# Optimization experiments

Measured on AMD Instinct MI355X. Metric: run time of the kernel, lower is better.

The kernel has to match this reference:

```python
import jax, jax.numpy as jnp
import numpy as np

V = 30522   # bert-base-uncased vocab size
B, S, D, J, K = 2, 512, 768, 12, 4
NUM_LABELS = 7


def setup_inputs() -> dict:
    key = jax.random.key(0)
    ks = jax.random.split(key, 9)
    return {
        "sequence_output": jax.random.normal(ks[0], (B, S, D), jnp.float32),
        "input_ids": jax.random.randint(ks[1], (B, S), 0, V),
        "neighbors": jax.random.randint(ks[2], (B, S, J, K), 0, V),
        "W_mlp": jax.random.normal(ks[3], (J * D, 13 * D), jnp.float32) * 0.02,
        "b_mlp": jnp.zeros((J * D,), jnp.float32),
        "W_attn": jax.random.normal(ks[4], (D, 2 * D), jnp.float32) * 0.02,
        "b_attn": jnp.zeros((D,), jnp.float32),
        "W_cls": jax.random.normal(ks[5], (NUM_LABELS, 2 * D), jnp.float32) * 0.02,
        "b_cls": jnp.zeros((NUM_LABELS,), jnp.float32),
    }


def _gather_neighbors(sequence_output, input_ids, neighbors):
    """Replicates the dict-based gather-sum. The torch dict persists ACROSS
    batch elements (it is never reset), with later positions overwriting
    earlier ones (last occurrence wins). We carry a [V,D] table + presence
    mask through a scan over the batch dim."""
    pos = jnp.arange(S, dtype=jnp.int32)

    def step(carry, xs):
        table, present = carry            # [V,D], [V] bool
        ids, seq, nb = xs                 # [S], [S,D], [S,J,K]
        # last occurrence index of each vocab id in this example (-1 if absent)
        last_idx = jnp.full((V,), -1, jnp.int32).at[ids].max(pos)
        found = last_idx >= 0
        table = jnp.where(found[:, None],
                          seq[jnp.clip(last_idx, 0, S - 1)], table)
        present = present | found
        # sum neighbor embeddings that are present in the dictionary
        emb = jnp.where(present[nb][..., None], table[nb], 0.0).sum(axis=2)  # [S,J,D]
        return (table, present), emb

    init = (jnp.zeros((V, D), sequence_output.dtype), jnp.zeros((V,), bool))
    _, fn = jax.lax.scan(step, init, (input_ids, sequence_output, neighbors))
    return fn                              # [B,S,J,D]


def reference(sequence_output, input_ids, neighbors,
              W_mlp, b_mlp, W_attn, b_attn, W_cls, b_cls):
    fn = _gather_neighbors(sequence_output, input_ids, neighbors)  # [B,S,J,D]
    n_flat = fn.reshape(B, S, J * D)
    # gated MLP: rij = [row ; neighbors], g = sigmoid(W rij), c' = g * n
    rij = jnp.concatenate([sequence_output, n_flat], axis=-1)      # [B,S,13D]
    g = jax.nn.sigmoid(jnp.einsum('bsf,gf->bsg', rij, W_mlp) + b_mlp)
    c = (g * n_flat).reshape(B, S, J, D)                           # [B,S,J,D]
    # Luong-style attention: query = token embedding, context = gated neighbors
    scores = jnp.einsum('bsd,bsjd->bsj', sequence_output, c)
    attn = jax.nn.softmax(scores, axis=-1)
    mix = jnp.einsum('bsj,bsjd->bsd', attn, c)                     # [B,S,D]
    combined = jnp.concatenate([mix, sequence_output], axis=-1)    # [B,S,2D]
    attn_out = jnp.tanh(jnp.einsum('bsf,df->bsd', combined, W_attn) + b_attn)
    final = jnp.concatenate([sequence_output, attn_out], axis=-1)  # [B,S,2D]
    # dropout is identity at inference
    logits = jnp.einsum('bsf,lf->bsl', final, W_cls) + b_cls       # [B,S,7]
    return logits
```

## Files before the change

kernel.cpp:

```cpp
#include <hip/hip_runtime.h>
#include <hip/hip_bf16.h>

#define V_PAD  30528
#define S_LEN  512
#define D_DIM  768
#define J_N    12
#define M_ROWS 1024
#define K_MLP  9984
#define N_MLP  9216
#define K_ATT  1536
#define N_ATT  768
#define N_LBL  7

using bf16x8 = __attribute__((ext_vector_type(8))) __bf16;
using f32x4  = __attribute__((ext_vector_type(4))) float;

__device__ __forceinline__ unsigned short f2bf(float f) {
  union { float f; unsigned int u; } c; c.f = f;
  unsigned int u = c.u;
  return (unsigned short)((u + 0x7fffu + ((u >> 16) & 1u)) >> 16);
}
__device__ __forceinline__ float bf2f(unsigned short h) {
  union { unsigned int u; float f; } c; c.u = (unsigned int)h << 16; return c.f;
}

__global__ __launch_bounds__(256)
void cvt_bf16_kernel(const float* __restrict__ in, unsigned short* __restrict__ out) {
  size_t i = (size_t)blockIdx.x * 256 + threadIdx.x;
  const float4 f0 = ((const float4*)in)[i * 2];
  const float4 f1 = ((const float4*)in)[i * 2 + 1];
  union { unsigned short h[8]; uint4 q; } pk;
  pk.h[0] = f2bf(f0.x); pk.h[1] = f2bf(f0.y); pk.h[2] = f2bf(f0.z); pk.h[3] = f2bf(f0.w);
  pk.h[4] = f2bf(f1.x); pk.h[5] = f2bf(f1.y); pk.h[6] = f2bf(f1.z); pk.h[7] = f2bf(f1.w);
  ((uint4*)out)[i] = pk.q;
}

__global__ void build_tables_kernel(const int* __restrict__ ids,
                                    int* __restrict__ last0,
                                    int* __restrict__ last01) {
  int p = blockIdx.x * 256 + threadIdx.x;
  if (p < M_ROWS) {
    int id = ids[p];
    atomicMax(&last01[id], p);
    if (p < S_LEN) atomicMax(&last0[id], p);
  }
}

__global__ __launch_bounds__(256) void seqrij_kernel(const float* __restrict__ seq,
                                                     unsigned short* __restrict__ rij) {
  int bs = blockIdx.x;
  for (int d = threadIdx.x; d < D_DIM; d += 256)
    rij[(size_t)bs * K_MLP + d] = f2bf(seq[(size_t)bs * D_DIM + d]);
}

template <bool WRITE_NFLAT>
__global__ __launch_bounds__(192)
void gather_kernel(const float* __restrict__ seq, const int* __restrict__ nbr,
                   const int* __restrict__ last0, const int* __restrict__ last01,
                   float* __restrict__ nflat, unsigned short* __restrict__ rij) {
  const int bsj = blockIdx.x;
  const int j  = bsj % J_N;
  const int bs = bsj / J_N;
  const int b  = bs >> 9;
  const int* nb = nbr + (size_t)bsj * 4;
  const int* tab = (b == 0) ? last0 : last01;
  const int s0 = tab[nb[0]], s1 = tab[nb[1]], s2 = tab[nb[2]], s3 = tab[nb[3]];
  const int d4 = threadIdx.x;
  float4 a = {0.f, 0.f, 0.f, 0.f};
  if (s0 >= 0) { float4 v = ((const float4*)(seq + (size_t)s0 * D_DIM))[d4]; a.x += v.x; a.y += v.y; a.z += v.z; a.w += v.w; }
  if (s1 >= 0) { float4 v = ((const float4*)(seq + (size_t)s1 * D_DIM))[d4]; a.x += v.x; a.y += v.y; a.z += v.z; a.w += v.w; }
  if (s2 >= 0) { float4 v = ((const float4*)(seq + (size_t)s2 * D_DIM))[d4]; a.x += v.x; a.y += v.y; a.z += v.z; a.w += v.w; }
  if (s3 >= 0) { float4 v = ((const float4*)(seq + (size_t)s3 * D_DIM))[d4]; a.x += v.x; a.y += v.y; a.z += v.z; a.w += v.w; }
  union { unsigned short h[4]; unsigned long long q; } pk;
  pk.h[0] = f2bf(a.x); pk.h[1] = f2bf(a.y); pk.h[2] = f2bf(a.z); pk.h[3] = f2bf(a.w);
  *(unsigned long long*)(rij + (size_t)bs * K_MLP + D_DIM + j * D_DIM + d4 * 4) = pk.q;
  if (WRITE_NFLAT)
    ((float4*)(nflat + (size_t)bs * N_MLP + j * D_DIM))[d4] = a;
}

template <int MODE, int TM, int TN, bool BF16B, bool SWZ>
__global__ __launch_bounds__(256)
void gemm_nt_kernel(const unsigned short* __restrict__ A,
                    const void* __restrict__ Wv,
                    const float* __restrict__ bias,
                    float* __restrict__ nflat_c,
                    float* __restrict__ outp,
                    int K, int N, int kchunk) {
  constexpr int FM = TM / 32;
  constexpr int FN = TN / 32;
  __shared__ unsigned short ldsA[2][TM * 32];
  __shared__ unsigned short ldsB[2][TN * 32];
  const int tid  = threadIdx.x;
  const int lane = tid & 63;
  const int w    = tid >> 6;

  int bx = blockIdx.x, by = blockIdx.y, bz = blockIdx.z;
  if (SWZ) {
    const unsigned l   = blockIdx.x + gridDim.x * (blockIdx.y + gridDim.y * blockIdx.z);
    const unsigned xcd = l & 7u;
    const unsigned c   = l >> 3;
    const unsigned gpx = (gridDim.y * gridDim.z) >> 3;
    const unsigned g   = xcd * gpx + c / gridDim.x;
    bx = (int)(c % gridDim.x);
    by = (int)(g % gridDim.y);
    bz = (int)(g / gridDim.y);
  }
  const int m0 = bx * TM;
  const int n0 = by * TN;
  const int kb = bz * kchunk;

  f32x4 acc[FM][FN];
#pragma unroll
  for (int i = 0; i < FM; ++i)
#pragma unroll
    for (int j = 0; j < FN; ++j) acc[i][j] = (f32x4){0.f, 0.f, 0.f, 0.f};

  const int lr  = lane >> 2;
  const int lcs = (((lane & 3) ^ ((lane >> 3) & 3)) * 8);
  const int wm = (w >> 1) * (TM / 2), wn = (w & 1) * (TN / 2);
  const int fr  = lane & 15;
  const int fc  = (((lane >> 4) ^ ((fr >> 1) & 3)) * 8);

  auto stage = [&](int buf, int kk) {
#pragma unroll
    for (int q = 0; q < TM / 64; ++q) {
      const int r = w * (TM / 4) + q * 16;
      const unsigned short* gsrc = A + (size_t)(m0 + r + lr) * K + kk + lcs;
      __builtin_amdgcn_global_load_lds(
          (const __attribute__((address_space(1))) void*)gsrc,
          (__attribute__((address_space(3))) void*)(&ldsA[buf][r * 32]), 16, 0, 0);
    }
    if (BF16B) {
#pragma unroll
      for (int q = 0; q < TN / 64; ++q) {
        const int r = w * (TN / 4) + q * 16;
        const unsigned short* gsrc = (const unsigned short*)Wv +
                                     (size_t)(n0 + r + lr) * K + kk + lcs;
        __builtin_amdgcn_global_load_lds(
            (const __attribute__((address_space(1))) void*)gsrc,
            (__attribute__((address_space(3))) void*)(&ldsB[buf][r * 32]), 16, 0, 0);
      }
    } else {
      constexpr int EPT = TN / 8;
      constexpr int TPR = 32 / EPT;
      const int br = tid / TPR, bc = (tid % TPR) * EPT;
      const float* gsrc = (const float*)Wv + (size_t)(n0 + br) * K + kk + bc;
      const int brs = (br >> 1) & 3;
#pragma unroll
      for (int e = 0; e < EPT; e += 8) {
        union { unsigned short h[8]; uint4 q4; } pk;
#pragma unroll
        for (int e2 = 0; e2 < 8; e2 += 4) {
          float4 f = *(const float4*)(gsrc + e + e2);
          pk.h[e2]     = f2bf(f.x); pk.h[e2 + 1] = f2bf(f.y);
          pk.h[e2 + 2] = f2bf(f.z); pk.h[e2 + 3] = f2bf(f.w);
        }
        const int slot = ((bc + e) >> 3) ^ brs;
        *(uint4*)&ldsB[buf][br * 32 + slot * 8] = pk.q4;
      }
    }
  };

  const int nt = kchunk >> 5;
  stage(0, kb);
  for (int t = 0; t < nt; ++t) {
    const int cur = t & 1;
    __syncthreads();
    if (t + 1 < nt) stage(cur ^ 1, kb + (t + 1) * 32);
    bf16x8 aF[FM], bF[FN];
#pragma unroll
    for (int i = 0; i < FM; ++i)
      aF[i] = *(const bf16x8*)&ldsA[cur][(wm + i * 16 + fr) * 32 + fc];
#pragma unroll
    for (int j = 0; j < FN; ++j)
      bF[j] = *(const bf16x8*)&ldsB[cur][(wn + j * 16 + fr) * 32 + fc];
#pragma unroll
    for (int i = 0; i < FM; ++i)
#pragma unroll
      for (int j = 0; j < FN; ++j)
        acc[i][j] = __builtin_amdgcn_mfma_f32_16x16x32_bf16(aF[i], bF[j], acc[i][j], 0, 0, 0);
  }

  const size_t zoff = (MODE == 2) ? (size_t)bz * M_ROWS * N : 0;
#pragma unroll
  for (int i = 0; i < FM; ++i) {
    int gm0 = m0 + wm + i * 16 + (lane >> 4) * 4;
#pragma unroll
    for (int j = 0; j < FN; ++j) {
      int gn = n0 + wn + j * 16 + (lane & 15);
      float bv = (MODE == 2) ? 0.f : bias[gn];
#pragma unroll
      for (int r = 0; r < 4; ++r) {
        size_t idx = (size_t)(gm0 + r) * N + gn;
        float x = acc[i][j][r] + bv;
        if (MODE == 0) {
          float gg = 1.0f / (1.0f + __expf(-x));
          nflat_c[idx] = gg * nflat_c[idx];
        } else if (MODE == 1) {
          outp[idx] = tanhf(x);
        } else {
          outp[zoff + idx] = x;
        }
      }
    }
  }
}

__global__ __launch_bounds__(256)
void attn_fused_kernel(const float* __restrict__ seq,
                       const float* __restrict__ p0, const float* __restrict__ p1,
                       const float* __restrict__ bmlp,
                       const unsigned short* __restrict__ rij,
                       unsigned short* __restrict__ combined) {
  __shared__ float sc[N_MLP];
  __shared__ float sq[D_DIM];
  __shared__ float ss[J_N];
  const int m = blockIdx.x;
  const int tid = threadIdx.x, lane = tid & 63, w = tid >> 6;
  for (int d = tid; d < D_DIM; d += 256) sq[d] = seq[(size_t)m * D_DIM + d];
  const float* q0 = p0 + (size_t)m * N_MLP;
  const float* q1 = p1 + (size_t)m * N_MLP;
  const unsigned short* nrow = rij + (size_t)m * K_MLP + D_DIM;
  for (int d = tid; d < N_MLP; d += 256) {
    float z = q0[d] + q1[d] + bmlp[d];
    float g = 1.0f / (1.0f + __expf(-z));
    sc[d] = g * bf2f(nrow[d]);
  }
  __syncthreads();
#pragma unroll
  for (int jj = 0; jj < 3; ++jj) {
    int j = w * 3 + jj;
    float p = 0.f;
    for (int d = lane; d < D_DIM; d += 64) p += sq[d] * sc[j * D_DIM + d];
#pragma unroll
    for (int off = 32; off > 0; off >>= 1) p += __shfl_down(p, off);
    if (lane == 0) ss[j] = p;
  }
  __syncthreads();
  float mx = ss[0];
#pragma unroll
  for (int j = 1; j < J_N; ++j) mx = fmaxf(mx, ss[j]);
  float aw[J_N]; float sum = 0.f;
#pragma unroll
  for (int j = 0; j < J_N; ++j) { aw[j] = __expf(ss[j] - mx); sum += aw[j]; }
  float inv = 1.f / sum;
  for (int d = tid; d < D_DIM; d += 256) {
    float mix = 0.f;
#pragma unroll
    for (int j = 0; j < J_N; ++j) mix += aw[j] * sc[j * D_DIM + d];
    combined[(size_t)m * K_ATT + d]         = f2bf(mix * inv);
    combined[(size_t)m * K_ATT + D_DIM + d] = f2bf(sq[d]);
  }
}

__global__ __launch_bounds__(256)
void attn_kernel(const float* __restrict__ seq, const float* __restrict__ c,
                 unsigned short* __restrict__ combined) {
  __shared__ float sc[N_MLP];
  __shared__ float sq[D_DIM];
  __shared__ float ss[J_N];
  const int m = blockIdx.x;
  const int tid = threadIdx.x, lane = tid & 63, w = tid >> 6;
  const float* crow = c + (size_t)m * N_MLP;
  for (int d = tid; d < N_MLP; d += 256) sc[d] = crow[d];
  for (int d = tid; d < D_DIM; d += 256) sq[d] = seq[(size_t)m * D_DIM + d];
  __syncthreads();
#pragma unroll
  for (int jj = 0; jj < 3; ++jj) {
    int j = w * 3 + jj;
    float p = 0.f;
    for (int d = lane; d < D_DIM; d += 64) p += sq[d] * sc[j * D_DIM + d];
#pragma unroll
    for (int off = 32; off > 0; off >>= 1) p += __shfl_down(p, off);
    if (lane == 0) ss[j] = p;
  }
  __syncthreads();
  float mx = ss[0];
#pragma unroll
  for (int j = 1; j < J_N; ++j) mx = fmaxf(mx, ss[j]);
  float aw[J_N]; float sum = 0.f;
#pragma unroll
  for (int j = 0; j < J_N; ++j) { aw[j] = __expf(ss[j] - mx); sum += aw[j]; }
  float inv = 1.f / sum;
  for (int d = tid; d < D_DIM; d += 256) {
    float mix = 0.f;
#pragma unroll
    for (int j = 0; j < J_N; ++j) mix += aw[j] * sc[j * D_DIM + d];
    combined[(size_t)m * K_ATT + d]         = f2bf(mix * inv);
    combined[(size_t)m * K_ATT + D_DIM + d] = f2bf(sq[d]);
  }
}

__global__ __launch_bounds__(256)
void cls_kernel(const float* __restrict__ seq, const float* __restrict__ attnout,
                const float* __restrict__ Wc, const float* __restrict__ bc,
                float* __restrict__ out) {
  __shared__ float part[4][N_LBL];
  const int m = blockIdx.x, tid = threadIdx.x, lane = tid & 63, w = tid >> 6;
  float p[N_LBL] = {0.f, 0.f, 0.f, 0.f, 0.f, 0.f, 0.f};
  for (int f = tid; f < K_ATT; f += 256) {
    float v = (f < D_DIM) ? seq[(size_t)m * D_DIM + f]
                          : attnout[(size_t)m * D_DIM + (f - D_DIM)];
#pragma unroll
    for (int l = 0; l < N_LBL; ++l) p[l] += v * Wc[l * K_ATT + f];
  }
#pragma unroll
  for (int l = 0; l < N_LBL; ++l) {
#pragma unroll
    for (int off = 32; off > 0; off >>= 1) p[l] += __shfl_down(p[l], off);
  }
  if (lane == 0) {
#pragma unroll
    for (int l = 0; l < N_LBL; ++l) part[w][l] = p[l];
  }
  __syncthreads();
  if (tid < N_LBL)
    out[(size_t)m * N_LBL + tid] =
        part[0][tid] + part[1][tid] + part[2][tid] + part[3][tid] + bc[tid];
}

extern "C" void kernel_launch(void* const* d_in, const int* in_sizes, int n_in,
                              void* d_out, int out_size, void* d_ws, size_t ws_size,
                              hipStream_t stream) {
  const float* seq   = (const float*)d_in[0];
  const int*   ids   = (const int*)d_in[1];
  const int*   nbr   = (const int*)d_in[2];
  const float* Wmlp  = (const float*)d_in[3];
  const float* bmlp  = (const float*)d_in[4];
  const float* Wattn = (const float*)d_in[5];
  const float* battn = (const float*)d_in[6];
  const float* Wcls  = (const float*)d_in[7];
  const float* bcls  = (const float*)d_in[8];
  float* out = (float*)d_out;

  char* ws = (char*)d_ws;
  size_t off = 0;
  int* last0  = (int*)(ws + off); off += (size_t)V_PAD * 4;
  int* last01 = (int*)(ws + off); off += (size_t)V_PAD * 4;
  unsigned short* rij = (unsigned short*)(ws + off); off += (size_t)M_ROWS * K_MLP * 2;
  unsigned short* combined = (unsigned short*)(ws + off); off += (size_t)M_ROWS * K_ATT * 2;
  float* attnout = (float*)(ws + off); off += (size_t)M_ROWS * N_ATT * 4;
  const size_t common = off;

  size_t ob = common;
  unsigned short* Wb_mlp  = (unsigned short*)(ws + ob); ob += (size_t)N_MLP * K_MLP * 2;
  unsigned short* Wb_attn = (unsigned short*)(ws + ob); ob += (size_t)N_ATT * K_ATT * 2;
  float* p0 = (float*)(ws + ob); ob += (size_t)M_ROWS * N_MLP * 4;
  float* p1 = (float*)(ws + ob); ob += (size_t)M_ROWS * N_MLP * 4;
  size_t om = common;
  float* nflat_m = (float*)(ws + om); om += (size_t)M_ROWS * N_MLP * 4;
  unsigned short* Wm_mlp  = (unsigned short*)(ws + om); om += (size_t)N_MLP * K_MLP * 2;
  unsigned short* Wm_attn = (unsigned short*)(ws + om); om += (size_t)N_ATT * K_ATT * 2;
  size_t os = common + (size_t)M_ROWS * N_MLP * 4;

  hipMemsetAsync(last0, 0xFF, (size_t)2 * V_PAD * 4, stream);
  build_tables_kernel<<<(M_ROWS + 255) / 256, 256, 0, stream>>>(ids, last0, last01);
  seqrij_kernel<<<M_ROWS, 256, 0, stream>>>(seq, rij);

  if (ws_size >= ob) {
    gather_kernel<false><<<M_ROWS * J_N, 192, 0, stream>>>(seq, nbr, last0, last01, nullptr, rij);
    cvt_bf16_kernel<<<(N_MLP * K_MLP) / (256 * 8), 256, 0, stream>>>(Wmlp, Wb_mlp);
    cvt_bf16_kernel<<<(N_ATT * K_ATT) / (256 * 8), 256, 0, stream>>>(Wattn, Wb_attn);
    gemm_nt_kernel<2, 128, 128, true, true><<<dim3(M_ROWS / 128, N_MLP / 128, 2), 256, 0, stream>>>(
        rij, Wb_mlp, nullptr, nullptr, p0, K_MLP, N_MLP, K_MLP / 2);
    attn_fused_kernel<<<M_ROWS, 256, 0, stream>>>(seq, p0, p1, bmlp, rij, combined);
    gemm_nt_kernel<1, 64, 64, true, false><<<dim3(M_ROWS / 64, N_ATT / 64), 256, 0, stream>>>(
        combined, Wb_attn, battn, nullptr, attnout, K_ATT, N_ATT, K_ATT);
  } else if (ws_size >= om) {
    gather_kernel<true><<<M_ROWS * J_N, 192, 0, stream>>>(seq, nbr, last0, last01, nflat_m, rij);
    cvt_bf16_kernel<<<(N_MLP * K_MLP) / (256 * 8), 256, 0, stream>>>(Wmlp, Wm_mlp);
    cvt_bf16_kernel<<<(N_ATT * K_ATT) / (256 * 8), 256, 0, stream>>>(Wattn, Wm_attn);
    gemm_nt_kernel<0, 128, 64, true, true><<<dim3(M_ROWS / 128, N_MLP / 64), 256, 0, stream>>>(
        rij, Wm_mlp, bmlp, nflat_m, nullptr, K_MLP, N_MLP, K_MLP);
    attn_kernel<<<M_ROWS, 256, 0, stream>>>(seq, nflat_m, combined);
    gemm_nt_kernel<1, 64, 64, true, false><<<dim3(M_ROWS / 64, N_ATT / 64), 256, 0, stream>>>(
        combined, Wm_attn, battn, nullptr, attnout, K_ATT, N_ATT, K_ATT);
  } else {
    float* nflat_s = nflat_m;
    (void)os;
    gather_kernel<true><<<M_ROWS * J_N, 192, 0, stream>>>(seq, nbr, last0, last01, nflat_s, rij);
    gemm_nt_kernel<0, 128, 64, false, true><<<dim3(M_ROWS / 128, N_MLP / 64), 256, 0, stream>>>(
        rij, Wmlp, bmlp, nflat_s, nullptr, K_MLP, N_MLP, K_MLP);
    attn_kernel<<<M_ROWS, 256, 0, stream>>>(seq, nflat_s, combined);
    gemm_nt_kernel<1, 64, 64, false, false><<<dim3(M_ROWS / 64, N_ATT / 64), 256, 0, stream>>>(
        combined, Wattn, battn, nullptr, attnout, K_ATT, N_ATT, K_ATT);
  }
  cls_kernel<<<M_ROWS, 256, 0, stream>>>(seq, attnout, Wcls, bcls, out);
}
```

Measured before the change: 861.0 us.

## Triple-buffer LDS staging with vmcnt waits and MFMA priority boost in GEMM

For the bf16-weight GEMM path, LDS staging moves from double to triple buffering, prefetching two k-tiles ahead. It replaces __syncthreads with explicit s_waitcnt vmcnt plus s_barrier so outstanding global loads can stay in flight across iterations. It also raises wave priority around the MFMA block with s_setprio. This is meant to hide global-load latency behind compute, at the cost of more shared memory, which may reduce occupancy. It also depends on the staging code issuing exactly the expected number of vector memory ops per stage.

Result: no change. 867.3 us (+0.7%).

```diff
diff --git a/kernel.cpp b/kernel.cpp
--- a/kernel.cpp
+++ b/kernel.cpp
@@ -22,6 +22,18 @@
 }
 __device__ __forceinline__ float bf2f(unsigned short h) {
   union { unsigned int u; float f; } c; c.u = (unsigned int)h << 16; return c.f;
+}
+
+template <int N>
+__device__ __forceinline__ void s_waitcnt_vmcnt() {
+  static_assert(N == 0 || N == 1 || N == 2 || N == 3 || N == 4 || N == 6 || N == 8, "");
+  if constexpr (N == 0) asm volatile("s_waitcnt vmcnt(0)" ::: "memory");
+  else if constexpr (N == 1) asm volatile("s_waitcnt vmcnt(1)" ::: "memory");
+  else if constexpr (N == 2) asm volatile("s_waitcnt vmcnt(2)" ::: "memory");
+  else if constexpr (N == 3) asm volatile("s_waitcnt vmcnt(3)" ::: "memory");
+  else if constexpr (N == 4) asm volatile("s_waitcnt vmcnt(4)" ::: "memory");
+  else if constexpr (N == 6) asm volatile("s_waitcnt vmcnt(6)" ::: "memory");
+  else if constexpr (N == 8) asm volatile("s_waitcnt vmcnt(8)" ::: "memory");
 }
 
 __global__ __launch_bounds__(256)
@@ -88,8 +100,9 @@
                     int K, int N, int kchunk) {
   constexpr int FM = TM / 32;
   constexpr int FN = TN / 32;
-  __shared__ unsigned short ldsA[2][TM * 32];
-  __shared__ unsigned short ldsB[2][TN * 32];
+  constexpr int LPS = TM / 64 + TN / 64;
+  __shared__ unsigned short ldsA[3][TM * 32];
+  __shared__ unsigned short ldsB[3][TN * 32];
   const int tid  = threadIdx.x;
   const int lane = tid & 63;
   const int w    = tid >> 6;
@@ -161,24 +174,43 @@
     }
   };
 
-  const int nt = kchunk >> 5;
-  stage(0, kb);
-  for (int t = 0; t < nt; ++t) {
-    const int cur = t & 1;
-    __syncthreads();
-    if (t + 1 < nt) stage(cur ^ 1, kb + (t + 1) * 32);
+  auto compute = [&](int buf) {
     bf16x8 aF[FM], bF[FN];
 #pragma unroll
     for (int i = 0; i < FM; ++i)
-      aF[i] = *(const bf16x8*)&ldsA[cur][(wm + i * 16 + fr) * 32 + fc];
+      aF[i] = *(const bf16x8*)&ldsA[buf][(wm + i * 16 + fr) * 32 + fc];
 #pragma unroll
     for (int j = 0; j < FN; ++j)
-      bF[j] = *(const bf16x8*)&ldsB[cur][(wn + j * 16 + fr) * 32 + fc];
+      bF[j] = *(const bf16x8*)&ldsB[buf][(wn + j * 16 + fr) * 32 + fc];
+    __builtin_amdgcn_s_setprio(1);
 #pragma unroll
     for (int i = 0; i < FM; ++i)
 #pragma unroll
       for (int j = 0; j < FN; ++j)
         acc[i][j] = __builtin_amdgcn_mfma_f32_16x16x32_bf16(aF[i], bF[j], acc[i][j], 0, 0, 0);
+    __builtin_amdgcn_s_setprio(0);
+  };
+
+  const int nt = kchunk >> 5;
+  if (BF16B) {
+    stage(0, kb);
+    if (nt > 1) stage(1, kb + 32);
+    int cur = 0;
+    for (int t = 0; t < nt; ++t) {
+      if (t + 1 < nt) s_waitcnt_vmcnt<LPS>(); else s_waitcnt_vmcnt<0>();
+      __builtin_amdgcn_s_barrier();
+      if (t + 2 < nt) stage(cur ? cur - 1 : 2, kb + (t + 2) * 32);
+      compute(cur);
+      cur = (cur == 2) ? 0 : cur + 1;
+    }
+  } else {
+    stage(0, kb);
+    for (int t = 0; t < nt; ++t) {
+      const int cur = t & 1;
+      __syncthreads();
+      if (t + 1 < nt) stage(cur ^ 1, kb + (t + 1) * 32);
+      compute(cur);
+    }
   }
 
   const size_t zoff = (MODE == 2) ? (size_t)bz * M_ROWS * N : 0;
```

## Fuse fp32 weight conversion and gating into MLP GEMM with register-prefetched B

Applied to the files above, without the earlier changes.

Removes the separate fp32-to-bf16 weight conversion kernels and the split-K MLP GEMM with its partial-sum buffers. The GEMM now loads fp32 weights into registers one tile ahead, converts them to bf16 into LDS, and applies the sigmoid gate times neighbour sums in the epilogue. Manual vmcnt waits, raw barriers and MFMA priority hints are added for pipelining. This trades the extra conversion pass and partial traffic for repeated fp32 weight reads per M-tile and fewer blocks without split-K.

Result: slower. 1.253 ms (+45.6%).

```diff
diff --git a/kernel.cpp b/kernel.cpp
--- a/kernel.cpp
+++ b/kernel.cpp
@@ -24,15 +24,14 @@
   union { unsigned int u; float f; } c; c.u = (unsigned int)h << 16; return c.f;
 }
 
-__global__ __launch_bounds__(256)
-void cvt_bf16_kernel(const float* __restrict__ in, unsigned short* __restrict__ out) {
-  size_t i = (size_t)blockIdx.x * 256 + threadIdx.x;
-  const float4 f0 = ((const float4*)in)[i * 2];
-  const float4 f1 = ((const float4*)in)[i * 2 + 1];
-  union { unsigned short h[8]; uint4 q; } pk;
-  pk.h[0] = f2bf(f0.x); pk.h[1] = f2bf(f0.y); pk.h[2] = f2bf(f0.z); pk.h[3] = f2bf(f0.w);
-  pk.h[4] = f2bf(f1.x); pk.h[5] = f2bf(f1.y); pk.h[6] = f2bf(f1.z); pk.h[7] = f2bf(f1.w);
-  ((uint4*)out)[i] = pk.q;
+template <int N>
+__device__ __forceinline__ void s_waitcnt_vmcnt() {
+  static_assert(N >= 0 && N <= 4, "");
+  if constexpr (N == 0) asm volatile("s_waitcnt vmcnt(0)" ::: "memory");
+  else if constexpr (N == 1) asm volatile("s_waitcnt vmcnt(1)" ::: "memory");
+  else if constexpr (N == 2) asm volatile("s_waitcnt vmcnt(2)" ::: "memory");
+  else if constexpr (N == 3) asm volatile("s_waitcnt vmcnt(3)" ::: "memory");
+  else if constexpr (N == 4) asm volatile("s_waitcnt vmcnt(4)" ::: "memory");
 }
 
 __global__ void build_tables_kernel(const int* __restrict__ ids,
@@ -53,11 +52,10 @@
     rij[(size_t)bs * K_MLP + d] = f2bf(seq[(size_t)bs * D_DIM + d]);
 }
 
-template <bool WRITE_NFLAT>
 __global__ __launch_bounds__(192)
 void gather_kernel(const float* __restrict__ seq, const int* __restrict__ nbr,
                    const int* __restrict__ last0, const int* __restrict__ last01,
-                   float* __restrict__ nflat, unsigned short* __restrict__ rij) {
+                   unsigned short* __restrict__ rij) {
   const int bsj = blockIdx.x;
   const int j  = bsj % J_N;
   const int bs = bsj / J_N;
@@ -74,40 +72,39 @@
   union { unsigned short h[4]; unsigned long long q; } pk;
   pk.h[0] = f2bf(a.x); pk.h[1] = f2bf(a.y); pk.h[2] = f2bf(a.z); pk.h[3] = f2bf(a.w);
   *(unsigned long long*)(rij + (size_t)bs * K_MLP + D_DIM + j * D_DIM + d4 * 4) = pk.q;
-  if (WRITE_NFLAT)
-    ((float4*)(nflat + (size_t)bs * N_MLP + j * D_DIM))[d4] = a;
-}
-
-template <int MODE, int TM, int TN, bool BF16B, bool SWZ>
+}
+
+template <int MODE, int TM, int TN, bool SWZ>
 __global__ __launch_bounds__(256)
 void gemm_nt_kernel(const unsigned short* __restrict__ A,
-                    const void* __restrict__ Wv,
+                    const float* __restrict__ Wf,
                     const float* __restrict__ bias,
-                    float* __restrict__ nflat_c,
                     float* __restrict__ outp,
-                    int K, int N, int kchunk) {
+                    int K, int N) {
   constexpr int FM = TM / 32;
   constexpr int FN = TN / 32;
+  constexpr int LPSA = TM / 64;
+  constexpr int EPT  = TN / 8;
+  constexpr int TPR  = 32 / EPT;
+  constexpr int NL4  = TN / 32;
+  constexpr int NCH  = EPT / 8;
   __shared__ unsigned short ldsA[2][TM * 32];
   __shared__ unsigned short ldsB[2][TN * 32];
   const int tid  = threadIdx.x;
   const int lane = tid & 63;
   const int w    = tid >> 6;
 
-  int bx = blockIdx.x, by = blockIdx.y, bz = blockIdx.z;
+  int bx = blockIdx.x, by = blockIdx.y;
   if (SWZ) {
-    const unsigned l   = blockIdx.x + gridDim.x * (blockIdx.y + gridDim.y * blockIdx.z);
+    const unsigned l   = blockIdx.x + gridDim.x * blockIdx.y;
     const unsigned xcd = l & 7u;
     const unsigned c   = l >> 3;
-    const unsigned gpx = (gridDim.y * gridDim.z) >> 3;
-    const unsigned g   = xcd * gpx + c / gridDim.x;
+    const unsigned gpx = gridDim.y >> 3;
+    by = (int)(xcd * gpx + c / gridDim.x);
     bx = (int)(c % gridDim.x);
-    by = (int)(g % gridDim.y);
-    bz = (int)(g / gridDim.y);
   }
   const int m0 = bx * TM;
   const int n0 = by * TN;
-  const int kb = bz * kchunk;
 
   f32x4 acc[FM][FN];
 #pragma unroll
@@ -121,7 +118,11 @@
   const int fr  = lane & 15;
   const int fc  = (((lane >> 4) ^ ((fr >> 1) & 3)) * 8);
 
-  auto stage = [&](int buf, int kk) {
+  const int br  = tid / TPR;
+  const int bc  = (tid % TPR) * EPT;
+  const int brs = (br >> 1) & 3;
+
+  auto stageA = [&](int buf, int kk) {
 #pragma unroll
     for (int q = 0; q < TM / 64; ++q) {
       const int r = w * (TM / 4) + q * 16;
@@ -130,126 +131,84 @@
           (const __attribute__((address_space(1))) void*)gsrc,
           (__attribute__((address_space(3))) void*)(&ldsA[buf][r * 32]), 16, 0, 0);
     }
-    if (BF16B) {
-#pragma unroll
-      for (int q = 0; q < TN / 64; ++q) {
-        const int r = w * (TN / 4) + q * 16;
-        const unsigned short* gsrc = (const unsigned short*)Wv +
-                                     (size_t)(n0 + r + lr) * K + kk + lcs;
-        __builtin_amdgcn_global_load_lds(
-            (const __attribute__((address_space(1))) void*)gsrc,
-            (__attribute__((address_space(3))) void*)(&ldsB[buf][r * 32]), 16, 0, 0);
-      }
-    } else {
-      constexpr int EPT = TN / 8;
-      constexpr int TPR = 32 / EPT;
-      const int br = tid / TPR, bc = (tid % TPR) * EPT;
-      const float* gsrc = (const float*)Wv + (size_t)(n0 + br) * K + kk + bc;
-      const int brs = (br >> 1) & 3;
-#pragma unroll
-      for (int e = 0; e < EPT; e += 8) {
-        union { unsigned short h[8]; uint4 q4; } pk;
-#pragma unroll
-        for (int e2 = 0; e2 < 8; e2 += 4) {
-          float4 f = *(const float4*)(gsrc + e + e2);
-          pk.h[e2]     = f2bf(f.x); pk.h[e2 + 1] = f2bf(f.y);
-          pk.h[e2 + 2] = f2bf(f.z); pk.h[e2 + 3] = f2bf(f.w);
-        }
-        const int slot = ((bc + e) >> 3) ^ brs;
-        *(uint4*)&ldsB[buf][br * 32 + slot * 8] = pk.q4;
-      }
+  };
+
+  float4 breg[NL4];
+  auto loadB = [&](int kk) {
+    const float4* g = (const float4*)(Wf + (size_t)(n0 + br) * K + kk + bc);
+#pragma unroll
+    for (int u = 0; u < NL4; ++u) breg[u] = g[u];
+  };
+  auto writeB = [&](int buf) {
+#pragma unroll
+    for (int ch = 0; ch < NCH; ++ch) {
+      union { unsigned short h[8]; uint4 q; } pk;
+      float4 f0 = breg[2 * ch], f1 = breg[2 * ch + 1];
+      pk.h[0] = f2bf(f0.x); pk.h[1] = f2bf(f0.y); pk.h[2] = f2bf(f0.z); pk.h[3] = f2bf(f0.w);
+      pk.h[4] = f2bf(f1.x); pk.h[5] = f2bf(f1.y); pk.h[6] = f2bf(f1.z); pk.h[7] = f2bf(f1.w);
+      const int slot = ((bc >> 3) + ch) ^ brs;
+      *(uint4*)&ldsB[buf][br * 32 + slot * 8] = pk.q;
     }
   };
 
-  const int nt = kchunk >> 5;
-  stage(0, kb);
+  auto compute = [&](int buf) {
+    bf16x8 aF[FM], bF[FN];
+#pragma unroll
+    for (int i = 0; i < FM; ++i)
+      aF[i] = *(const bf16x8*)&ldsA[buf][(wm + i * 16 + fr) * 32 + fc];
+#pragma unroll
+    for (int j = 0; j < FN; ++j)
+      bF[j] = *(const bf16x8*)&ldsB[buf][(wn + j * 16 + fr) * 32 + fc];
+    __builtin_amdgcn_s_setprio(1);
+#pragma unroll
+    for (int i = 0; i < FM; ++i)
+#pragma unroll
+      for (int j = 0; j < FN; ++j)
+        acc[i][j] = __builtin_amdgcn_mfma_f32_16x16x32_bf16(aF[i], bF[j], acc[i][j], 0, 0, 0);
+    __builtin_amdgcn_s_setprio(0);
+  };
+
+  const int nt = K >> 5;
+  loadB(0);
+  s_waitcnt_vmcnt<0>();
+  writeB(0);
+  stageA(0, 0);
+  loadB(32);
   for (int t = 0; t < nt; ++t) {
     const int cur = t & 1;
-    __syncthreads();
-    if (t + 1 < nt) stage(cur ^ 1, kb + (t + 1) * 32);
-    bf16x8 aF[FM], bF[FN];
-#pragma unroll
-    for (int i = 0; i < FM; ++i)
-      aF[i] = *(const bf16x8*)&ldsA[cur][(wm + i * 16 + fr) * 32 + fc];
-#pragma unroll
-    for (int j = 0; j < FN; ++j)
-      bF[j] = *(const bf16x8*)&ldsB[cur][(wn + j * 16 + fr) * 32 + fc];
-#pragma unroll
-    for (int i = 0; i < FM; ++i)
-#pragma unroll
-      for (int j = 0; j < FN; ++j)
-        acc[i][j] = __builtin_amdgcn_mfma_f32_16x16x32_bf16(aF[i], bF[j], acc[i][j], 0, 0, 0);
-  }
-
-  const size_t zoff = (MODE == 2) ? (size_t)bz * M_ROWS * N : 0;
+    if (t + 1 < nt) s_waitcnt_vmcnt<NL4>(); else s_waitcnt_vmcnt<0>();
+    asm volatile("s_waitcnt lgkmcnt(0)" ::: "memory");
+    __builtin_amdgcn_s_barrier();
+    __builtin_amdgcn_sched_barrier(0);
+    if (t + 1 < nt) {
+      stageA(cur ^ 1, (t + 1) * 32);
+      s_waitcnt_vmcnt<LPSA>();
+      writeB(cur ^ 1);
+      if (t + 2 < nt) loadB((t + 2) * 32);
+    }
+    compute(cur);
+  }
+
 #pragma unroll
   for (int i = 0; i < FM; ++i) {
     int gm0 = m0 + wm + i * 16 + (lane >> 4) * 4;
 #pragma unroll
     for (int j = 0; j < FN; ++j) {
       int gn = n0 + wn + j * 16 + (lane & 15);
-      float bv = (MODE == 2) ? 0.f : bias[gn];
+      float bv = bias[gn];
 #pragma unroll
       for (int r = 0; r < 4; ++r) {
         size_t idx = (size_t)(gm0 + r) * N + gn;
         float x = acc[i][j][r] + bv;
-        if (MODE == 0) {
+        if (MODE == 3) {
           float gg = 1.0f / (1.0f + __expf(-x));
-          nflat_c[idx] = gg * nflat_c[idx];
-        } else if (MODE == 1) {
+          float nv = bf2f(A[(size_t)(gm0 + r) * K + D_DIM + gn]);
+          outp[idx] = gg * nv;
+        } else {
           outp[idx] = tanhf(x);
-        } else {
-          outp[zoff + idx] = x;
         }
       }
     }
-  }
-}
-
-__global__ __launch_bounds__(256)
-void attn_fused_kernel(const float* __restrict__ seq,
-                       const float* __restrict__ p0, const float* __restrict__ p1,
-                       const float* __restrict__ bmlp,
-                       const unsigned short* __restrict__ rij,
-                       unsigned short* __restrict__ combined) {
-  __shared__ float sc[N_MLP];
-  __shared__ float sq[D_DIM];
-  __shared__ float ss[J_N];
-  const int m = blockIdx.x;
-  const int tid = threadIdx.x, lane = tid & 63, w = tid >> 6;
-  for (int d = tid; d < D_DIM; d += 256) sq[d] = seq[(size_t)m * D_DIM + d];
-  const float* q0 = p0 + (size_t)m * N_MLP;
-  const float* q1 = p1 + (size_t)m * N_MLP;
-  const unsigned short* nrow = rij + (size_t)m * K_MLP + D_DIM;
-  for (int d = tid; d < N_MLP; d += 256) {
-    float z = q0[d] + q1[d] + bmlp[d];
-    float g = 1.0f / (1.0f + __expf(-z));
-    sc[d] = g * bf2f(nrow[d]);
-  }
-  __syncthreads();
-#pragma unroll
-  for (int jj = 0; jj < 3; ++jj) {
-    int j = w * 3 + jj;
-    float p = 0.f;
-    for (int d = lane; d < D_DIM; d += 64) p += sq[d] * sc[j * D_DIM + d];
-#pragma unroll
-    for (int off = 32; off > 0; off >>= 1) p += __shfl_down(p, off);
-    if (lane == 0) ss[j] = p;
-  }
-  __syncthreads();
-  float mx = ss[0];
-#pragma unroll
-  for (int j = 1; j < J_N; ++j) mx = fmaxf(mx, ss[j]);
-  float aw[J_N]; float sum = 0.f;
-#pragma unroll
-  for (int j = 0; j < J_N; ++j) { aw[j] = __expf(ss[j] - mx); sum += aw[j]; }
-  float inv = 1.f / sum;
-  for (int d = tid; d < D_DIM; d += 256) {
-    float mix = 0.f;
-#pragma unroll
-    for (int j = 0; j < J_N; ++j) mix += aw[j] * sc[j * D_DIM + d];
-    combined[(size_t)m * K_ATT + d]         = f2bf(mix * inv);
-    combined[(size_t)m * K_ATT + D_DIM + d] = f2bf(sq[d]);
   }
 }
 
@@ -332,6 +291,7 @@
   const float* Wcls  = (const float*)d_in[7];
   const float* bcls  = (const float*)d_in[8];
   float* out = (float*)d_out;
+  (void)in_sizes; (void)n_in; (void)out_size; (void)ws_size;
 
   char* ws = (char*)d_ws;
   size_t off = 0;
@@ -340,50 +300,17 @@
   unsigned short* rij = (unsigned short*)(ws + off); off += (size_t)M_ROWS * K_MLP * 2;
   unsigned short* combined = (unsigned short*)(ws + off); off += (size_t)M_ROWS * K_ATT * 2;
   float* attnout = (float*)(ws + off); off += (size_t)M_ROWS * N_ATT * 4;
-  const size_t common = off;
-
-  size_t ob = common;
-  unsigned short* Wb_mlp  = (unsigned short*)(ws + ob); ob += (size_t)N_MLP * K_MLP * 2;
-  unsigned short* Wb_attn = (unsigned short*)(ws + ob); ob += (size_t)N_ATT * K_ATT * 2;
-  float* p0 = (float*)(ws + ob); ob += (size_t)M_ROWS * N_MLP * 4;
-  float* p1 = (float*)(ws + ob); ob += (size_t)M_ROWS * N_MLP * 4;
-  size_t om = common;
-  float* nflat_m = (float*)(ws + om); om += (size_t)M_ROWS * N_MLP * 4;
-  unsigned short* Wm_mlp  = (unsigned short*)(ws + om); om += (size_t)N_MLP * K_MLP * 2;
-  unsigned short* Wm_attn = (unsigned short*)(ws + om); om += (size_t)N_ATT * K_ATT * 2;
-  size_t os = common + (size_t)M_ROWS * N_MLP * 4;
+  float* cgate   = (float*)(ws + off); off += (size_t)M_ROWS * N_MLP * 4;
 
   hipMemsetAsync(last0, 0xFF, (size_t)2 * V_PAD * 4, stream);
   build_tables_kernel<<<(M_ROWS + 255) / 256, 256, 0, stream>>>(ids, last0, last01);
   seqrij_kernel<<<M_ROWS, 256, 0, stream>>>(seq, rij);
-
-  if (ws_size >= ob) {
-    gather_kernel<false><<<M_ROWS * J_N, 192, 0, stream>>>(seq, nbr, last0, last01, nullptr, rij);
-    cvt_bf16_kernel<<<(N_MLP * K_MLP) / (256 * 8), 256, 0, stream>>>(Wmlp, Wb_mlp);
-    cvt_bf16_kernel<<<(N_ATT * K_ATT) / (256 * 8), 256, 0, stream>>>(Wattn, Wb_attn);
-    gemm_nt_kernel<2, 128, 128, true, true><<<dim3(M_ROWS / 128, N_MLP / 128, 2), 256, 0, stream>>>(
-        rij, Wb_mlp, nullptr, nullptr, p0, K_MLP, N_MLP, K_MLP / 2);
-    attn_fused_kernel<<<M_ROWS, 256, 0, stream>>>(seq, p0, p1, bmlp, rij, combined);
-    gemm_nt_kernel<1, 64, 64, true, false><<<dim3(M_ROWS / 64, N_ATT / 64), 256, 0, stream>>>(
-        combined, Wb_attn, battn, nullptr, attnout, K_ATT, N_ATT, K_ATT);
-  } else if (ws_size >= om) {
-    gather_kernel<true><<<M_ROWS * J_N, 192, 0, stream>>>(seq, nbr, last0, last01, nflat_m, rij);
-    cvt_bf16_kernel<<<(N_MLP * K_MLP) / (256 * 8), 256, 0, stream>>>(Wmlp, Wm_mlp);
-    cvt_bf16_kernel<<<(N_ATT * K_ATT) / (256 * 8), 256, 0, stream>>>(Wattn, Wm_attn);
-    gemm_nt_kernel<0, 128, 64, true, true><<<dim3(M_ROWS / 128, N_MLP / 64), 256, 0, stream>>>(
-        rij, Wm_mlp, bmlp, nflat_m, nullptr, K_MLP, N_MLP, K_MLP);
-    attn_kernel<<<M_ROWS, 256, 0, stream>>>(seq, nflat_m, combined);
-    gemm_nt_kernel<1, 64, 64, true, false><<<dim3(M_ROWS / 64, N_ATT / 64), 256, 0, stream>>>(
-        combined, Wm_attn, battn, nullptr, attnout, K_ATT, N_ATT, K_ATT);
-  } else {
-    float* nflat_s = nflat_m;
-    (void)os;
-    gather_kernel<true><<<M_ROWS * J_N, 192, 0, stream>>>(seq, nbr, last0, last01, nflat_s, rij);
-    gemm_nt_kernel<0, 128, 64, false, true><<<dim3(M_ROWS / 128, N_MLP / 64), 256, 0, stream>>>(
-        rij, Wmlp, bmlp, nflat_s, nullptr, K_MLP, N_MLP, K_MLP);
-    attn_kernel<<<M_ROWS, 256, 0, stream>>>(seq, nflat_s, combined);
-    gemm_nt_kernel<1, 64, 64, false, false><<<dim3(M_ROWS / 64, N_ATT / 64), 256, 0, stream>>>(
-        combined, Wattn, battn, nullptr, attnout, K_ATT, N_ATT, K_ATT);
-  }
+  gather_kernel<<<M_ROWS * J_N, 192, 0, stream>>>(seq, nbr, last0, last01, rij);
+
+  gemm_nt_kernel<3, 128, 128, true><<<dim3(M_ROWS / 128, N_MLP / 128), 256, 0, stream>>>(
+      rij, Wmlp, bmlp, cgate, K_MLP, N_MLP);
+  attn_kernel<<<M_ROWS, 256, 0, stream>>>(seq, cgate, combined);
+  gemm_nt_kernel<1, 64, 64, false><<<dim3(M_ROWS / 64, N_ATT / 64), 256, 0, stream>>>(
+      combined, Wattn, battn, attnout, K_ATT, N_ATT);
   cls_kernel<<<M_ROWS, 256, 0, stream>>>(seq, attnout, Wcls, bcls, out);
 }
```
